# Optimization experiments

Hardware: AMD Instinct MI355X
Metric: run time of the kernel (lower is better)

The kernel has to match this reference:

```python
import jax, jax.numpy as jnp
import numpy as np

N_NODES = 100000
N_EDGES = 3200000
IN_DIM = 128
OUT_DIM = 128
BN_EPS = 1e-5
FILL_VALUE = 1.0  # improved_gcn=False -> self-loop weight 1.0 (2.0 if improved)


def setup_inputs() -> dict:
    key = jax.random.key(0)
    k1, k2, k3, k4 = jax.random.split(key, 4)
    node_features = jax.random.normal(k1, (N_NODES, IN_DIM), dtype=jnp.float32)
    edge_index = jax.random.randint(k2, (2, N_EDGES), 0, N_NODES, dtype=jnp.int64)
    edge_weight = jax.random.uniform(k3, (N_EDGES,), dtype=jnp.float32)
    # Glorot init like PyG GCNConv
    W = jax.random.normal(k4, (IN_DIM, OUT_DIM), dtype=jnp.float32) * np.sqrt(2.0 / (IN_DIM + OUT_DIM))
    b = jnp.zeros((OUT_DIM,), dtype=jnp.float32)
    gamma = jnp.ones((OUT_DIM,), dtype=jnp.float32)
    beta = jnp.zeros((OUT_DIM,), dtype=jnp.float32)
    return {"node_features": node_features, "edge_index": edge_index,
            "edge_weight": edge_weight, "W": W, "b": b, "gamma": gamma, "beta": beta}


def reference(node_features, edge_index, edge_weight, W, b, gamma, beta):
    N = node_features.shape[0]
    dt = node_features.dtype
    # --- gcn_norm: add self loops, symmetric normalization ---
    loop = jnp.arange(N, dtype=edge_index.dtype)
    row = jnp.concatenate([edge_index[0], loop])  # source
    col = jnp.concatenate([edge_index[1], loop])  # target (aggregation dim)
    w = jnp.concatenate([edge_weight.astype(dt), jnp.full((N,), FILL_VALUE, dtype=dt)])
    deg = jax.ops.segment_sum(w, col, num_segments=N)
    dinv = jnp.where(deg > 0, jax.lax.rsqrt(deg), 0.0).astype(dt)
    norm = dinv[row] * w * dinv[col]  # [E+N]
    # --- linear transform then message passing (scatter-add into targets) ---
    x = node_features @ W  # [N, out_dim]
    msg = x[row] * norm[:, None]  # [E+N, out_dim] gather
    out = jax.ops.segment_sum(msg, col, num_segments=N) + b
    # --- relu ---
    h = jax.nn.relu(out)
    # --- BatchNorm1d (training-mode batch statistics, biased variance) ---
    mean = jnp.mean(h, axis=0)
    var = jnp.mean(jnp.square(h - mean), axis=0)
    h = (h - mean) * jax.lax.rsqrt(var + BN_EPS) * gamma + beta
    # dropout is identity in eval / deterministic reference
    return h
```

## Files before the change

kernel.cpp:

```cpp
#include <hip/hip_runtime.h>
#include <hip/hip_bf16.h>


#define BKT_BITS 7
#define BKT_SZ 128
#define MAX_BKT 1024
#define CHUNK 8192

typedef __attribute__((ext_vector_type(8))) short bf16x8;
typedef __attribute__((ext_vector_type(4))) float f32x4;

__device__ __forceinline__ unsigned bf16rn(float f) {
    unsigned x = __float_as_uint(f);
    return (x + 0x7fffu + ((x >> 16) & 1u)) >> 16;
}
__device__ __forceinline__ float bflo(unsigned u) { return __uint_as_float(u << 16); }
__device__ __forceinline__ float bfhi(unsigned u) { return __uint_as_float(u & 0xffff0000u); }

__global__ __launch_bounds__(256) void k_bhist2(const int* __restrict__ col,
        int* __restrict__ blkoff, int E, int nb, int nbc) {
    __shared__ int h[MAX_BKT];
    for (int i = threadIdx.x; i < nb; i += 256) h[i] = 0;
    __syncthreads();
    int base = blockIdx.x * CHUNK, lim = min(base + CHUNK, E);
    for (int e = base + threadIdx.x; e < lim; e += 256)
        atomicAdd(&h[col[e] >> BKT_BITS], 1);
    __syncthreads();
    for (int i = threadIdx.x; i < nb; i += 256)
        blkoff[(size_t)i * nbc + blockIdx.x] = h[i];
}

__global__ void k_bscan2a(int* __restrict__ blkoff, int* __restrict__ btot,
                          int nb, int nbc) {
    int b = blockIdx.x * 256 + threadIdx.x;
    if (b >= nb) return;
    int* p = blkoff + (size_t)b * nbc;
    int run = 0;
#pragma unroll 4
    for (int i = 0; i < nbc; ++i) { int c = p[i]; p[i] = run; run += c; }
    btot[b] = run;
}

__global__ __launch_bounds__(1024) void k_bscan2b(const int* __restrict__ btot,
        int* __restrict__ bbase, int* __restrict__ ptr, float* __restrict__ sums,
        int nb, int N, int E) {
    __shared__ int ls[1024];
    int t = threadIdx.x;
    int v = (t < nb) ? btot[t] : 0;
    ls[t] = v;
    __syncthreads();
    for (int off = 1; off < 1024; off <<= 1) {
        int u = (t >= off) ? ls[t - off] : 0;
        __syncthreads();
        ls[t] += u;
        __syncthreads();
    }
    if (t < nb) bbase[t] = ls[t] - v;
    if (t == nb - 1) bbase[nb] = ls[t];
    if (t == 0) ptr[N] = E;
    if (t < 512) sums[t] = 0.0f;
}

__global__ __launch_bounds__(256) void k_passA3(
        const int* __restrict__ row, const int* __restrict__ col,
        const float* __restrict__ w, const int* __restrict__ blkoff,
        const int* __restrict__ bbase, int2* __restrict__ tmp,
        int E, int nb, int nbc) {
    __shared__ int cur[MAX_BKT];
    for (int i = threadIdx.x; i < nb; i += 256)
        cur[i] = bbase[i] + blkoff[(size_t)i * nbc + blockIdx.x];
    __syncthreads();
    int base = blockIdx.x * CHUNK, lim = min(base + CHUNK, E);
    for (int e = base + threadIdx.x; e < lim; e += 256) {
        int c = col[e];
        int pos = atomicAdd(&cur[c >> BKT_BITS], 1);
        tmp[pos] = make_int2(row[e] | ((c & (BKT_SZ - 1)) << 17), __float_as_int(w[e]));
    }
}

__global__ __launch_bounds__(256) void k_passB2(
        const int2* __restrict__ tmp, const int* __restrict__ bbase,
        unsigned* __restrict__ packed, int* __restrict__ ptr,
        float* __restrict__ dinv, int N) {
    __shared__ int hcnt[BKT_SZ];
    __shared__ float wsum[BKT_SZ];
    __shared__ int cur[BKT_SZ];
    int b = blockIdx.x;
    int t = threadIdx.x;
    if (t < BKT_SZ) { hcnt[t] = 0; wsum[t] = 0.0f; }
    __syncthreads();
    int beg = bbase[b], end = bbase[b + 1];
    for (int k = beg + t; k < end; k += 256) {
        int2 p = tmp[k];
        int li = (p.x >> 17) & (BKT_SZ - 1);
        atomicAdd(&hcnt[li], 1);
        atomicAdd(&wsum[li], __int_as_float(p.y));
    }
    __syncthreads();
    if (t < BKT_SZ) cur[t] = hcnt[t];
    __syncthreads();
    for (int off = 1; off < BKT_SZ; off <<= 1) {
        int v = (t < BKT_SZ && t >= off) ? cur[t - off] : 0;
        __syncthreads();
        if (t < BKT_SZ) cur[t] += v;
        __syncthreads();
    }
    if (t < BKT_SZ) {
        int p = beg + cur[t] - hcnt[t];
        cur[t] = p;
        int n = (b << BKT_BITS) + t;
        if (n < N) {
            ptr[n] = p;
            float d = 1.0f + wsum[t];
            dinv[n] = d > 0.0f ? rsqrtf(d) : 0.0f;
        }
    }
    __syncthreads();
    for (int k = beg + t; k < end; k += 256) {
        int2 p = tmp[k];
        int li = (p.x >> 17) & (BKT_SZ - 1);
        int pos = atomicAdd(&cur[li], 1);
        float wf = __int_as_float(p.y);
        int q = (int)(wf * 32768.0f + 0.5f);
        q = q > 32767 ? 32767 : (q < 0 ? 0 : q);
        packed[pos] = ((unsigned)(p.x & 0x1FFFF) << 15) | (unsigned)q;
    }
}

__global__ void k_conv2(const float* __restrict__ nf, const float* __restrict__ dinv,
                        uint4* __restrict__ tab, int N) {
    size_t i = (size_t)blockIdx.x * 256 + threadIdx.x;
    if (i >= (size_t)N * 16) return;
    int n = (int)(i >> 4);
    float dv = dinv[n];
    const float4* src = (const float4*)nf + 2 * i;
    float4 a = src[0], b = src[1];
    uint4 r;
    r.x = bf16rn(a.x * dv) | (bf16rn(a.y * dv) << 16);
    r.y = bf16rn(a.z * dv) | (bf16rn(a.w * dv) << 16);
    r.z = bf16rn(b.x * dv) | (bf16rn(b.y * dv) << 16);
    r.w = bf16rn(b.z * dv) | (bf16rn(b.w * dv) << 16);
    tab[i] = r;
}

__global__ void k_convW(const float* __restrict__ W, unsigned* __restrict__ WT) {
    int i = blockIdx.x * 256 + threadIdx.x;
    if (i >= 128 * 64) return;
    int j = i >> 6, w = i & 63;
    float a = W[(size_t)(2 * w) * 128 + j];
    float b = W[(size_t)(2 * w + 1) * 128 + j];
    WT[i] = bf16rn(a) | (bf16rn(b) << 16);
}

#define EDGE_FMA(aX, nX, tX)                                     \
    aX[0] += nX * bflo(tX.x); aX[1] += nX * bfhi(tX.x);          \
    aX[2] += nX * bflo(tX.y); aX[3] += nX * bfhi(tX.y);          \
    aX[4] += nX * bflo(tX.z); aX[5] += nX * bfhi(tX.z);          \
    aX[6] += nX * bflo(tX.w); aX[7] += nX * bfhi(tX.w);

__global__ __launch_bounds__(256) void k_gatherw4(
        const unsigned* __restrict__ packed, const int* __restrict__ ptr,
        const float* __restrict__ dinv, const unsigned* __restrict__ tab,
        unsigned* __restrict__ aggb, int N) {
    int wid = (int)(((size_t)blockIdx.x * 256 + threadIdx.x) >> 6);
    int lane = threadIdx.x & 63;
    if (wid >= N) return;
    int beg = ptr[wid], end = ptr[wid + 1];
    float dc = dinv[wid];
    float dcq = dc * (1.0f / 32768.0f);
    int q = lane >> 4;
    int fl = lane & 15;
    float a0[8] = {}, a1[8] = {}, a2[8] = {}, a3[8] = {};
    for (int k = beg; k < end; k += 16) {
        int i0 = k + q, i1 = k + 4 + q, i2 = k + 8 + q, i3 = k + 12 + q;
        unsigned p0 = packed[i0 < end ? i0 : beg];
        unsigned p1 = packed[i1 < end ? i1 : beg];
        unsigned p2 = packed[i2 < end ? i2 : beg];
        unsigned p3 = packed[i3 < end ? i3 : beg];
        float n0 = i0 < end ? dcq * (float)(p0 & 0x7FFF) : 0.0f;
        float n1 = i1 < end ? dcq * (float)(p1 & 0x7FFF) : 0.0f;
        float n2 = i2 < end ? dcq * (float)(p2 & 0x7FFF) : 0.0f;
        float n3 = i3 < end ? dcq * (float)(p3 & 0x7FFF) : 0.0f;
        uint4 t0 = *(const uint4*)(tab + (size_t)(p0 >> 15) * 64 + fl * 4);
        uint4 t1 = *(const uint4*)(tab + (size_t)(p1 >> 15) * 64 + fl * 4);
        uint4 t2 = *(const uint4*)(tab + (size_t)(p2 >> 15) * 64 + fl * 4);
        uint4 t3 = *(const uint4*)(tab + (size_t)(p3 >> 15) * 64 + fl * 4);
        EDGE_FMA(a0, n0, t0)
        EDGE_FMA(a1, n1, t1)
        EDGE_FMA(a2, n2, t2)
        EDGE_FMA(a3, n3, t3)
    }
#pragma unroll
    for (int j = 0; j < 8; ++j) {
        float s = (a0[j] + a1[j]) + (a2[j] + a3[j]);
        s += __shfl_xor(s, 16);
        s += __shfl_xor(s, 32);
        a0[j] = s;
    }
    if (q == 0) {
        uint4 t = *(const uint4*)(tab + (size_t)wid * 64 + fl * 4);
        EDGE_FMA(a0, dc, t)
        uint4 r;
        r.x = bf16rn(a0[0]) | (bf16rn(a0[1]) << 16);
        r.y = bf16rn(a0[2]) | (bf16rn(a0[3]) << 16);
        r.z = bf16rn(a0[4]) | (bf16rn(a0[5]) << 16);
        r.w = bf16rn(a0[6]) | (bf16rn(a0[7]) << 16);
        *(uint4*)(aggb + (size_t)wid * 64 + fl * 4) = r;
    }
}

__global__ __launch_bounds__(256) void k_gatherwF(
        const unsigned* __restrict__ packed, const int* __restrict__ ptr,
        const float* __restrict__ dinv, const unsigned* __restrict__ tab,
        float* __restrict__ out, int N) {
    int wid = (int)(((size_t)blockIdx.x * 256 + threadIdx.x) >> 6);
    int lane = threadIdx.x & 63;
    if (wid >= N) return;
    int beg = ptr[wid], end = ptr[wid + 1];
    float dc = dinv[wid];
    float dcq = dc * (1.0f / 32768.0f);
    int q = lane >> 4;
    int fl = lane & 15;
    float a0[8] = {}, a1[8] = {};
    for (int k = beg; k < end; k += 8) {
        int i0 = k + q, i1 = k + 4 + q;
        unsigned p0 = packed[i0 < end ? i0 : beg];
        unsigned p1 = packed[i1 < end ? i1 : beg];
        float n0 = i0 < end ? dcq * (float)(p0 & 0x7FFF) : 0.0f;
        float n1 = i1 < end ? dcq * (float)(p1 & 0x7FFF) : 0.0f;
        uint4 t0 = *(const uint4*)(tab + (size_t)(p0 >> 15) * 64 + fl * 4);
        uint4 t1 = *(const uint4*)(tab + (size_t)(p1 >> 15) * 64 + fl * 4);
        EDGE_FMA(a0, n0, t0)
        EDGE_FMA(a1, n1, t1)
    }
#pragma unroll
    for (int j = 0; j < 8; ++j) {
        float s = a0[j] + a1[j];
        s += __shfl_xor(s, 16);
        s += __shfl_xor(s, 32);
        a0[j] = s;
    }
    if (q == 0) {
        uint4 t = *(const uint4*)(tab + (size_t)wid * 64 + fl * 4);
        EDGE_FMA(a0, dc, t)
        float4* dst = (float4*)(out + (size_t)wid * 128 + fl * 8);
        dst[0] = make_float4(a0[0], a0[1], a0[2], a0[3]);
        dst[1] = make_float4(a0[4], a0[5], a0[6], a0[7]);
    }
}

__global__ __launch_bounds__(256) void k_gemm3b(
        unsigned* aggb, const unsigned* __restrict__ WT,
        const float* __restrict__ bias, float* __restrict__ sums, int N) {
    __shared__ unsigned A_l[128][68];
    __shared__ unsigned W_l[128][68];
    __shared__ float bs[256];
    int tid = threadIdx.x;
    int r0 = blockIdx.x * 128;
    bs[tid] = 0.0f;
    {
        int j = tid >> 1, h = tid & 1;
        const uint4* src = (const uint4*)(WT + j * 64 + h * 32);
#pragma unroll
        for (int i = 0; i < 8; ++i)
            *(uint4*)&W_l[j][h * 32 + i * 4] = src[i];
    }
    {
        int j = tid >> 1, h = tid & 1;
        int gr = r0 + j;
        if (gr < N) {
            const uint4* src = (const uint4*)(aggb + (size_t)gr * 64 + h * 32);
#pragma unroll
            for (int i = 0; i < 8; ++i)
                *(uint4*)&A_l[j][h * 32 + i * 4] = src[i];
        } else {
            uint4 z = {0, 0, 0, 0};
#pragma unroll
            for (int i = 0; i < 8; ++i)
                *(uint4*)&A_l[j][h * 32 + i * 4] = z;
        }
    }
    __syncthreads();

    int wv = tid >> 6, l = tid & 63;
    int lr = l & 15, lk = l >> 4;
    f32x4 acc[2][8] = {};
#pragma unroll
    for (int ks = 0; ks < 4; ++ks) {
        bf16x8 a0 = *(bf16x8*)&A_l[wv * 32 + lr][ks * 16 + lk * 4];
        bf16x8 a1 = *(bf16x8*)&A_l[wv * 32 + 16 + lr][ks * 16 + lk * 4];
#pragma unroll
        for (int nt = 0; nt < 8; ++nt) {
            bf16x8 b = *(bf16x8*)&W_l[nt * 16 + lr][ks * 16 + lk * 4];
            acc[0][nt] = __builtin_amdgcn_mfma_f32_16x16x32_bf16(a0, b, acc[0][nt], 0, 0, 0);
            acc[1][nt] = __builtin_amdgcn_mfma_f32_16x16x32_bf16(a1, b, acc[1][nt], 0, 0, 0);
        }
    }

    unsigned short* ab = (unsigned short*)aggb;
#pragma unroll
    for (int nt = 0; nt < 8; ++nt) {
        int colc = nt * 16 + lr;
        float bc = bias[colc];
        float s = 0.0f, sq = 0.0f;
#pragma unroll
        for (int ms = 0; ms < 2; ++ms) {
#pragma unroll
            for (int p = 0; p < 4; ++p) {
                int rrow = r0 + wv * 32 + ms * 16 + lk * 4 + p;
                float v = fmaxf(acc[ms][nt][p] + bc, 0.0f);
                if (rrow < N) {
                    ab[(size_t)rrow * 128 + colc] = (unsigned short)bf16rn(v);
                    s += v;
                    sq += v * v;
                }
            }
        }
        s += __shfl_xor(s, 16);  s += __shfl_xor(s, 32);
        sq += __shfl_xor(sq, 16); sq += __shfl_xor(sq, 32);
        if (l < 16) {
            atomicAdd(&bs[colc], s);
            atomicAdd(&bs[128 + colc], sq);
        }
    }
    __syncthreads();
    if (tid < 128) {
        atomicAdd(&sums[tid], bs[tid]);
        atomicAdd(&sums[128 + tid], bs[128 + tid]);
    }
}

__global__ void k_bnfin(float* __restrict__ sums, const float* __restrict__ gamma,
                        const float* __restrict__ beta, int N) {
    int j = threadIdx.x;
    float inv_n = 1.0f / (float)N;
    float mean = sums[j] * inv_n;
    float var = sums[128 + j] * inv_n - mean * mean;
    float sc = rsqrtf(var + 1e-5f) * gamma[j];
    sums[256 + j] = sc;
    sums[384 + j] = beta[j] - mean * sc;
}

__global__ void k_bnapplyB(const unsigned* __restrict__ aggb,
                           const float* __restrict__ sums,
                           float* __restrict__ out, size_t n16) {
    size_t i = (size_t)blockIdx.x * 256 + threadIdx.x;
    if (i >= n16) return;
    int g = (int)(i & 15);
    uint4 v = ((const uint4*)aggb)[i];
    float4 sc0 = *(const float4*)(sums + 256 + g * 8);
    float4 sc1 = *(const float4*)(sums + 256 + g * 8 + 4);
    float4 sh0 = *(const float4*)(sums + 384 + g * 8);
    float4 sh1 = *(const float4*)(sums + 384 + g * 8 + 4);
    float4 o0, o1;
    o0.x = bflo(v.x) * sc0.x + sh0.x;
    o0.y = bfhi(v.x) * sc0.y + sh0.y;
    o0.z = bflo(v.y) * sc0.z + sh0.z;
    o0.w = bfhi(v.y) * sc0.w + sh0.w;
    o1.x = bflo(v.z) * sc1.x + sh1.x;
    o1.y = bfhi(v.z) * sc1.y + sh1.y;
    o1.z = bflo(v.w) * sc1.z + sh1.z;
    o1.w = bfhi(v.w) * sc1.w + sh1.w;
    ((float4*)out)[2 * i] = o0;
    ((float4*)out)[2 * i + 1] = o1;
}

__global__ void k_bnapply(float* __restrict__ h, const float* __restrict__ sums, size_t n4) {
    size_t i = (size_t)blockIdx.x * 256 + threadIdx.x;
    if (i >= n4) return;
    int j4 = (int)(i & 31);
    float4 v = ((float4*)h)[i];
    float4 sc = ((const float4*)(sums + 256))[j4];
    float4 sh = ((const float4*)(sums + 384))[j4];
    v.x = v.x * sc.x + sh.x;
    v.y = v.y * sc.y + sh.y;
    v.z = v.z * sc.z + sh.z;
    v.w = v.w * sc.w + sh.w;
    ((float4*)h)[i] = v;
}

__global__ void k_init0(int* __restrict__ bcnt, float* __restrict__ sums, int nb) {
    int i = blockIdx.x * 256 + threadIdx.x;
    if (i < nb) bcnt[i] = 0;
    if (blockIdx.x == 0 && threadIdx.x < 512) sums[threadIdx.x] = 0.0f;
}
__global__ __launch_bounds__(256) void k_bhist(const int* __restrict__ col,
                                               int* __restrict__ bcnt, int E, int nb) {
    __shared__ int h[MAX_BKT];
    for (int i = threadIdx.x; i < nb; i += 256) h[i] = 0;
    __syncthreads();
    int base = blockIdx.x * CHUNK, lim = min(base + CHUNK, E);
    for (int e = base + threadIdx.x; e < lim; e += 256)
        atomicAdd(&h[col[e] >> BKT_BITS], 1);
    __syncthreads();
    for (int i = threadIdx.x; i < nb; i += 256) {
        int c = h[i];
        if (c) atomicAdd(&bcnt[i], c);
    }
}
__global__ __launch_bounds__(1024) void k_bscan(const int* __restrict__ bcnt,
        int* __restrict__ bbase, int* __restrict__ bcur,
        int* __restrict__ ptr, int nb, int N, int E) {
    __shared__ int ls[1024];
    int t = threadIdx.x;
    int v = (t < nb) ? bcnt[t] : 0;
    ls[t] = v;
    __syncthreads();
    for (int off = 1; off < 1024; off <<= 1) {
        int u = (t >= off) ? ls[t - off] : 0;
        __syncthreads();
        ls[t] += u;
        __syncthreads();
    }
    if (t < nb) {
        int ex = ls[t] - v;
        bbase[t] = ex;
        bcur[t] = ex;
    }
    if (t == nb - 1) bbase[nb] = ls[t];
    if (t == 0) ptr[N] = E;
}
__global__ __launch_bounds__(256) void k_passA2(
        const int* __restrict__ row, const int* __restrict__ col,
        const float* __restrict__ w, int* __restrict__ bcur,
        int2* __restrict__ tmp, int E, int nb) {
    __shared__ int h[MAX_BKT];
    for (int i = threadIdx.x; i < nb; i += 256) h[i] = 0;
    __syncthreads();
    int base = blockIdx.x * CHUNK, lim = min(base + CHUNK, E);
    for (int e = base + threadIdx.x; e < lim; e += 256)
        atomicAdd(&h[col[e] >> BKT_BITS], 1);
    __syncthreads();
    for (int i = threadIdx.x; i < nb; i += 256) {
        int c = h[i];
        if (c) h[i] = atomicAdd(&bcur[i], c);
    }
    __syncthreads();
    for (int e = base + threadIdx.x; e < lim; e += 256) {
        int c = col[e];
        int b = c >> BKT_BITS;
        int pos = atomicAdd(&h[b], 1);
        tmp[pos] = make_int2(row[e] | ((c & (BKT_SZ - 1)) << 17), __float_as_int(w[e]));
    }
}

__global__ void k_init(int* __restrict__ cnt, float* __restrict__ sums, int N) {
    int i = blockIdx.x * 256 + threadIdx.x;
    if (i < N) cnt[i] = 0;
    if (blockIdx.x == 0 && threadIdx.x < 512) sums[threadIdx.x] = 0.0f;
}
__global__ void k_count(const int* __restrict__ col, int* __restrict__ cnt, int E) {
    int e = blockIdx.x * 256 + threadIdx.x;
    if (e < E) atomicAdd(&cnt[col[e]], 1);
}
__global__ __launch_bounds__(256) void kS1(const int* __restrict__ cnt,
                                           int* __restrict__ ptr,
                                           int* __restrict__ bsum, int N) {
    __shared__ int ls[256];
    int t = threadIdx.x, i = blockIdx.x * 256 + t;
    int v = (i < N) ? cnt[i] : 0;
    ls[t] = v;
    __syncthreads();
    for (int off = 1; off < 256; off <<= 1) {
        int u = (t >= off) ? ls[t - off] : 0;
        __syncthreads();
        ls[t] += u;
        __syncthreads();
    }
    if (i < N) ptr[i] = ls[t] - v;
    if (t == 255) bsum[blockIdx.x] = ls[255];
}
__global__ __launch_bounds__(512) void kS2(int* __restrict__ bsum,
                                           int* __restrict__ ptr, int NB, int N) {
    __shared__ int ls[512];
    int t = threadIdx.x;
    int chunk = (NB + 511) / 512;
    int b = t * chunk, e = min(b + chunk, NB);
    int s = 0;
    for (int i = b; i < e; ++i) s += bsum[i];
    ls[t] = s;
    __syncthreads();
    for (int off = 1; off < 512; off <<= 1) {
        int u = (t >= off) ? ls[t - off] : 0;
        __syncthreads();
        ls[t] += u;
        __syncthreads();
    }
    int run = ls[t] - s;
    for (int i = b; i < e; ++i) { int c = bsum[i]; bsum[i] = run; run += c; }
    if (t == 511) ptr[N] = ls[511];
}
__global__ void kS3(int* __restrict__ ptr, int* __restrict__ cnt,
                    const int* __restrict__ bsum, int N) {
    int i = blockIdx.x * 256 + threadIdx.x;
    if (i >= N) return;
    int p = ptr[i] + bsum[blockIdx.x];
    ptr[i] = p;
    cnt[i] = p;
}
__global__ void k_fill(const int* __restrict__ row, const int* __restrict__ col,
                       const float* __restrict__ w, int* __restrict__ cursor,
                       int2* __restrict__ packed, int E) {
    int e = blockIdx.x * 256 + threadIdx.x;
    if (e < E) {
        int pos = atomicAdd(&cursor[col[e]], 1);
        packed[pos] = make_int2(row[e], __float_as_int(w[e]));
    }
}
__global__ __launch_bounds__(256) void k_degw(const int2* __restrict__ packed,
                                              const int* __restrict__ ptr,
                                              float* __restrict__ dinv, int N) {
    int wid = (int)(((size_t)blockIdx.x * 256 + threadIdx.x) >> 6);
    int lane = threadIdx.x & 63;
    if (wid >= N) return;
    int beg = ptr[wid], end = ptr[wid + 1];
    float s = 0.0f;
    for (int k = beg + lane; k < end; k += 64) s += __int_as_float(packed[k].y);
#pragma unroll
    for (int off = 32; off; off >>= 1) s += __shfl_xor(s, off);
    if (lane == 0) {
        float d = 1.0f + s;
        dinv[wid] = d > 0.0f ? rsqrtf(d) : 0.0f;
    }
}
__global__ __launch_bounds__(256) void k_gather(
        const int2* __restrict__ packed, const int* __restrict__ ptr,
        const float* __restrict__ dinv, const float* __restrict__ nf,
        float* __restrict__ out, int N) {
    int wid = (int)(((size_t)blockIdx.x * 256 + threadIdx.x) >> 6);
    int lane = threadIdx.x & 63;
    if (wid >= N) return;
    int c = wid;
    int beg = ptr[c], end = ptr[c + 1];
    float dc = dinv[c];
    int half = lane >> 5;
    int fl = lane & 31;
    float4 acc = {0.f, 0.f, 0.f, 0.f};
    for (int k = beg; k < end; k += 2) {
        int idx = k + half;
        bool v = idx < end;
        int2 p = packed[v ? idx : beg];
        float nrm = v ? dc * __int_as_float(p.y) * dinv[p.x] : 0.0f;
        float4 x = ((const float4*)(nf + (size_t)p.x * 128))[fl];
        acc.x += nrm * x.x; acc.y += nrm * x.y;
        acc.z += nrm * x.z; acc.w += nrm * x.w;
    }
    acc.x += __shfl_xor(acc.x, 32);
    acc.y += __shfl_xor(acc.y, 32);
    acc.z += __shfl_xor(acc.z, 32);
    acc.w += __shfl_xor(acc.w, 32);
    if (half == 0) {
        float s2 = dc * dc;
        float4 sf = ((const float4*)(nf + (size_t)c * 128))[fl];
        acc.x += s2 * sf.x; acc.y += s2 * sf.y;
        acc.z += s2 * sf.z; acc.w += s2 * sf.w;
        ((float4*)(out + (size_t)c * 128))[fl] = acc;
    }
}
__global__ void k_initA(float* __restrict__ deg, float* __restrict__ sums, int N) {
    int i = blockIdx.x * 256 + threadIdx.x;
    if (i < N) deg[i] = 1.0f;
    if (blockIdx.x == 0 && threadIdx.x < 512) sums[threadIdx.x] = 0.0f;
}
__global__ void k_deg(const int* __restrict__ col, const float* __restrict__ w,
                      float* __restrict__ deg, int E) {
    int e = blockIdx.x * 256 + threadIdx.x;
    if (e < E) atomicAdd(&deg[col[e]], w[e]);
}
__global__ void k_dinv(float* __restrict__ deg, int N) {
    int i = blockIdx.x * 256 + threadIdx.x;
    if (i < N) { float d = deg[i]; deg[i] = d > 0.0f ? rsqrtf(d) : 0.0f; }
}
__global__ void k_self(const float* __restrict__ nf, const float* __restrict__ dinv,
                       float* __restrict__ agg, int N) {
    size_t i = (size_t)blockIdx.x * 256 + threadIdx.x;
    if (i >= (size_t)N * 32) return;
    int node = (int)(i >> 5);
    float s = dinv[node]; s = s * s;
    float4 v = ((const float4*)nf)[i];
    v.x *= s; v.y *= s; v.z *= s; v.w *= s;
    ((float4*)agg)[i] = v;
}
__global__ __launch_bounds__(256) void k_scatter(
        const int* __restrict__ row, const int* __restrict__ col,
        const float* __restrict__ w, const float* __restrict__ dinv,
        const float* __restrict__ nf, float* __restrict__ agg, int E) {
    int wid = (int)(((size_t)blockIdx.x * blockDim.x + threadIdx.x) >> 6);
    int lane = threadIdx.x & 63;
    if (wid >= E) return;
    int r = row[wid], c = col[wid];
    float nrm = dinv[r] * w[wid] * dinv[c];
    float2 v = ((const float2*)(nf + (size_t)r * 128))[lane];
    float* dst = agg + (size_t)c * 128 + lane * 2;
    atomicAdd(dst, v.x * nrm);
    atomicAdd(dst + 1, v.y * nrm);
}

__global__ __launch_bounds__(256) void k_gemm2(float* __restrict__ h,
        const float* __restrict__ W, const float* __restrict__ bias,
        float* __restrict__ sums, int N) {
    __shared__ float At[2][32][132];
    __shared__ float Wt[2][32][132];
    int tid = threadIdx.x;
    int tx = tid & 15, ty = tid >> 4;
    int r0 = blockIdx.x * 128;
#define STAGE_A(buf, k0)                                                     \
    _Pragma("unroll")                                                        \
    for (int i = 0; i < 4; ++i) {                                            \
        int idx = tid + 256 * i;                                             \
        int row = idx >> 3, c4 = idx & 7;                                    \
        int gr = r0 + row; if (gr > N - 1) gr = N - 1;                       \
        float4 v = *(const float4*)&h[(size_t)gr * 128 + (k0) + c4 * 4];     \
        At[buf][c4 * 4 + 0][row] = v.x;                                      \
        At[buf][c4 * 4 + 1][row] = v.y;                                      \
        At[buf][c4 * 4 + 2][row] = v.z;                                      \
        At[buf][c4 * 4 + 3][row] = v.w;                                      \
    }
#define STAGE_W(buf, k0)                                                     \
    _Pragma("unroll")                                                        \
    for (int i = 0; i < 4; ++i) {                                            \
        int idx = tid + 256 * i;                                             \
        int kk = idx >> 5, c4 = idx & 31;                                    \
        float4 v = *(const float4*)&W[(size_t)((k0) + kk) * 128 + c4 * 4];   \
        *(float4*)&Wt[buf][kk][c4 * 4] = v;                                  \
    }
    STAGE_A(0, 0)
    STAGE_W(0, 0)
    float acc[8][8] = {};
    for (int t = 0; t < 4; ++t) {
        __syncthreads();
        if (t < 3) {
            int nb = (t + 1) & 1;
            STAGE_A(nb, (t + 1) * 32)
            STAGE_W(nb, (t + 1) * 32)
        }
        int kb = t & 1;
#pragma unroll
        for (int k = 0; k < 32; ++k) {
            float a[8], w[8];
            *(float4*)&a[0] = *(float4*)&At[kb][k][ty * 8];
            *(float4*)&a[4] = *(float4*)&At[kb][k][ty * 8 + 4];
            *(float4*)&w[0] = *(float4*)&Wt[kb][k][tx * 8];
            *(float4*)&w[4] = *(float4*)&Wt[kb][k][tx * 8 + 4];
#pragma unroll
            for (int r = 0; r < 8; ++r)
#pragma unroll
                for (int cc = 0; cc < 8; ++cc)
                    acc[r][cc] += a[r] * w[cc];
        }
    }
    float bv[8];
    *(float4*)&bv[0] = *(const float4*)&bias[tx * 8];
    *(float4*)&bv[4] = *(const float4*)&bias[tx * 8 + 4];
    float s[8] = {}, sq[8] = {};
#pragma unroll
    for (int r = 0; r < 8; ++r) {
        int gr = r0 + ty * 8 + r;
        if (gr < N) {
            float o[8];
#pragma unroll
            for (int cc = 0; cc < 8; ++cc) {
                o[cc] = fmaxf(acc[r][cc] + bv[cc], 0.0f);
                s[cc] += o[cc];
                sq[cc] += o[cc] * o[cc];
            }
            float4* dst = (float4*)&h[(size_t)gr * 128 + tx * 8];
            dst[0] = make_float4(o[0], o[1], o[2], o[3]);
            dst[1] = make_float4(o[4], o[5], o[6], o[7]);
        }
    }
    float* ls = &At[0][0][0];
    __syncthreads();
#pragma unroll
    for (int cc = 0; cc < 8; ++cc) {
        ls[ty * 128 + tx * 8 + cc] = s[cc];
        ls[2048 + ty * 128 + tx * 8 + cc] = sq[cc];
    }
    __syncthreads();
    if (tid < 128) {
        float ssum = 0.f, sqsum = 0.f;
#pragma unroll
        for (int u = 0; u < 16; ++u) {
            ssum += ls[u * 128 + tid];
            sqsum += ls[2048 + u * 128 + tid];
        }
        atomicAdd(&sums[tid], ssum);
        atomicAdd(&sums[128 + tid], sqsum);
    }
#undef STAGE_A
#undef STAGE_W
}

extern "C" void kernel_launch(void* const* d_in, const int* in_sizes, int n_in,
                              void* d_out, int out_size, void* d_ws, size_t ws_size,
                              hipStream_t stream) {
    const float* nf    = (const float*)d_in[0];
    const int*   ei    = (const int*)d_in[1];
    const float* ew    = (const float*)d_in[2];
    const float* W     = (const float*)d_in[3];
    const float* bias  = (const float*)d_in[4];
    const float* gamma = (const float*)d_in[5];
    const float* beta  = (const float*)d_in[6];
    float* out = (float*)d_out;

    const int N = in_sizes[0] / 128;
    const int E = in_sizes[2];
    const int* row = ei;
    const int* col = ei + E;

    int nb_n  = (N + 255) / 256;
    int nb_e  = (E + 255) / 256;
    int nb_w  = (int)(((size_t)N + 3) / 4);
    int nb_v4 = (int)(((size_t)N * 32 + 255) / 256);
    int nbk   = (N + BKT_SZ - 1) >> BKT_BITS;
    int nb_c  = (E + CHUNK - 1) / CHUNK;
    int nconv = (int)(((size_t)N * 16 + 255) / 256);
    size_t n16 = (size_t)N * 16;
    size_t tt_words = (size_t)64 * N > (size_t)2 * E ? (size_t)64 * N : (size_t)2 * E;

    float* dinv = (float*)d_ws;
    int*   ptr  = (int*)d_ws + N;
    float* sums = (float*)d_ws + 2 * N + 1;
    int*   bbase1 = (int*)d_ws + 2 * N + 513;
    int*   btot   = bbase1 + nbk + 1;
    int*   blkoff = btot + nbk;
    size_t wt_off = ((size_t)(2 * N + 514 + 2 * nbk) + (size_t)nbk * nb_c + 3) & ~(size_t)3;
    unsigned* wtb = (unsigned*)((int*)d_ws + wt_off);
    size_t pk_off = (wt_off + 8192 + 3) & ~(size_t)3;
    unsigned* p1_packed = (unsigned*)((int*)d_ws + pk_off);
    size_t tt_off = (pk_off + (size_t)E + 3) & ~(size_t)3;
    int2*  p1_tmp = (int2*)((int*)d_ws + tt_off);
    unsigned* p1_tab = (unsigned*)((int*)d_ws + tt_off);
    size_t ab_off = (tt_off + tt_words + 3) & ~(size_t)3;
    unsigned* aggb = (unsigned*)((int*)d_ws + ab_off);
    size_t need_p1 = (ab_off + (size_t)64 * N) * 4;

    float* dinv2 = (float*)d_ws;
    int*   ptr2  = (int*)d_ws + N;
    int*   cnt3  = (int*)d_ws + 2 * N + 1;
    float* sums2 = (float*)d_ws + 3 * N + 1;
    int*   bsum2 = (int*)d_ws + 3 * N + 513;
    int*   bbase2 = (int*)d_ws + 3 * N + 1025;
    int*   bcur2  = bbase2 + nbk + 1;
    size_t pk2 = ((size_t)(3 * N + 1026 + 2 * nbk) + 3) & ~(size_t)3;
    int2*  packed2 = (int2*)((int*)d_ws + pk2);
    size_t tt2 = (pk2 + (size_t)2 * E + 3) & ~(size_t)3;
    int2*  tmp2 = (int2*)((int*)d_ws + tt2);
    unsigned* tab2 = (unsigned*)((int*)d_ws + tt2);
    size_t need_csr2  = tt2 * 4;
    size_t need_full2 = (tt2 + tt_words) * 4;

    if (nbk <= MAX_BKT && ws_size >= need_p1) {
        k_convW<<<32, 256, 0, stream>>>(W, wtb);
        k_bhist2<<<nb_c, 256, 0, stream>>>(col, blkoff, E, nbk, nb_c);
        k_bscan2a<<<(nbk + 255) / 256, 256, 0, stream>>>(blkoff, btot, nbk, nb_c);
        k_bscan2b<<<1, 1024, 0, stream>>>(btot, bbase1, ptr, sums, nbk, N, E);
        k_passA3<<<nb_c, 256, 0, stream>>>(row, col, ew, blkoff, bbase1, p1_tmp, E, nbk, nb_c);
        k_passB2<<<nbk, 256, 0, stream>>>(p1_tmp, bbase1, p1_packed, ptr, dinv, N);
        k_conv2<<<nconv, 256, 0, stream>>>(nf, dinv, (uint4*)p1_tab, N);
        k_gatherw4<<<nb_w, 256, 0, stream>>>(p1_packed, ptr, dinv, p1_tab, aggb, N);
        k_gemm3b<<<(N + 127) / 128, 256, 0, stream>>>(aggb, wtb, bias, sums, N);
        k_bnfin<<<1, 128, 0, stream>>>(sums, gamma, beta, N);
        k_bnapplyB<<<(int)((n16 + 255) / 256), 256, 0, stream>>>(aggb, sums, out, n16);
        return;
    }

    if (nbk <= MAX_BKT && ws_size >= need_full2) {
        k_init0<<<(max(nbk, 512) + 255) / 256, 256, 0, stream>>>(bcur2, sums2, nbk);
        k_bhist<<<nb_c, 256, 0, stream>>>(col, bcur2, E, nbk);
        k_bscan<<<1, 1024, 0, stream>>>(bcur2, bbase2, bcur2, ptr2, nbk, N, E);
        k_passA2<<<nb_c, 256, 0, stream>>>(row, col, ew, bcur2, tmp2, E, nbk);
        k_passB2<<<nbk, 256, 0, stream>>>(tmp2, bbase2, (unsigned*)packed2, ptr2, dinv2, N);
        k_conv2<<<nconv, 256, 0, stream>>>(nf, dinv2, (uint4*)tab2, N);
        k_gatherwF<<<nb_w, 256, 0, stream>>>((unsigned*)packed2, ptr2, dinv2, tab2, out, N);
        k_gemm2<<<(N + 127) / 128, 256, 0, stream>>>(out, W, bias, sums2, N);
        k_bnfin<<<1, 128, 0, stream>>>(sums2, gamma, beta, N);
        k_bnapply<<<nb_v4, 256, 0, stream>>>(out, sums2, (size_t)N * 32);
        return;
    }

    if (ws_size >= need_csr2) {
        k_init<<<nb_n, 256, 0, stream>>>(cnt3, sums2, N);
        k_count<<<nb_e, 256, 0, stream>>>(col, cnt3, E);
        kS1<<<nb_n, 256, 0, stream>>>(cnt3, ptr2, bsum2, N);
        kS2<<<1, 512, 0, stream>>>(bsum2, ptr2, nb_n, N);
        kS3<<<nb_n, 256, 0, stream>>>(ptr2, cnt3, bsum2, N);
        k_fill<<<nb_e, 256, 0, stream>>>(row, col, ew, cnt3, packed2, E);
        k_degw<<<nb_w, 256, 0, stream>>>(packed2, ptr2, dinv2, N);
        k_gather<<<nb_w, 256, 0, stream>>>(packed2, ptr2, dinv2, nf, out, N);
        k_gemm2<<<(N + 127) / 128, 256, 0, stream>>>(out, W, bias, sums2, N);
        k_bnfin<<<1, 128, 0, stream>>>(sums2, gamma, beta, N);
        k_bnapply<<<nb_v4, 256, 0, stream>>>(out, sums2, (size_t)N * 32);
        return;
    }

    {
        float* deg = (float*)d_ws;
        float* sm  = (float*)d_ws + N;
        k_initA<<<nb_n, 256, 0, stream>>>(deg, sm, N);
        k_deg<<<nb_e, 256, 0, stream>>>(col, ew, deg, E);
        k_dinv<<<nb_n, 256, 0, stream>>>(deg, N);
        k_self<<<nb_v4, 256, 0, stream>>>(nf, deg, out, N);
        k_scatter<<<(E + 3) / 4, 256, 0, stream>>>(row, col, ew, deg, nf, out, E);
        k_gemm2<<<(N + 127) / 128, 256, 0, stream>>>(out, W, bias, sm, N);
        k_bnfin<<<1, 128, 0, stream>>>(sm, gamma, beta, N);
        k_bnapply<<<nb_v4, 256, 0, stream>>>(out, sm, (size_t)N * 32);
    }
}
```

Baseline: 352.4 us.

## Pack edge records into 32-bit words and fold dinv into per-edge weights

The intermediate bucket record shrinks from an int2 (row, local col, float weight) to a single 32-bit word holding the row, the local column and an 8-bit quantized weight. This halves the scatter and reread traffic in passA/passB. passB now folds the target's dinv into the 15-bit packed norm, so the gather no longer multiplies by dc per edge. The gather loops are restructured into full unrolled blocks plus a remainder, which removes the per-edge bounds predication. Quantizing edge weights to 8 bits loses precision in both the degree and the norm, and the row<<15 packing limits row indices to 17 bits.

```diff
diff --git a/kernel.cpp b/kernel.cpp
--- a/kernel.cpp
+++ b/kernel.cpp
@@ -64,7 +64,7 @@
 __global__ __launch_bounds__(256) void k_passA3(
         const int* __restrict__ row, const int* __restrict__ col,
         const float* __restrict__ w, const int* __restrict__ blkoff,
-        const int* __restrict__ bbase, int2* __restrict__ tmp,
+        const int* __restrict__ bbase, unsigned* __restrict__ tmp,
         int E, int nb, int nbc) {
     __shared__ int cur[MAX_BKT];
     for (int i = threadIdx.x; i < nb; i += 256)
@@ -73,28 +73,32 @@
     int base = blockIdx.x * CHUNK, lim = min(base + CHUNK, E);
     for (int e = base + threadIdx.x; e < lim; e += 256) {
         int c = col[e];
+        int q8 = (int)(w[e] * 256.0f + 0.5f);
+        if (q8 > 255) q8 = 255;
+        unsigned rec = ((unsigned)row[e] << 15) | ((unsigned)(c & 127) << 8) | (unsigned)q8;
         int pos = atomicAdd(&cur[c >> BKT_BITS], 1);
-        tmp[pos] = make_int2(row[e] | ((c & (BKT_SZ - 1)) << 17), __float_as_int(w[e]));
+        tmp[pos] = rec;
     }
 }
 
 __global__ __launch_bounds__(256) void k_passB2(
-        const int2* __restrict__ tmp, const int* __restrict__ bbase,
+        const unsigned* __restrict__ tmp, const int* __restrict__ bbase,
         unsigned* __restrict__ packed, int* __restrict__ ptr,
         float* __restrict__ dinv, int N) {
     __shared__ int hcnt[BKT_SZ];
-    __shared__ float wsum[BKT_SZ];
+    __shared__ int wsumi[BKT_SZ];
     __shared__ int cur[BKT_SZ];
+    __shared__ float dcl[BKT_SZ];
     int b = blockIdx.x;
     int t = threadIdx.x;
-    if (t < BKT_SZ) { hcnt[t] = 0; wsum[t] = 0.0f; }
+    if (t < BKT_SZ) { hcnt[t] = 0; wsumi[t] = 0; }
     __syncthreads();
     int beg = bbase[b], end = bbase[b + 1];
     for (int k = beg + t; k < end; k += 256) {
-        int2 p = tmp[k];
-        int li = (p.x >> 17) & (BKT_SZ - 1);
+        unsigned p = tmp[k];
+        int li = (p >> 8) & 127;
         atomicAdd(&hcnt[li], 1);
-        atomicAdd(&wsum[li], __int_as_float(p.y));
+        atomicAdd(&wsumi[li], (int)(p & 255u));
     }
     __syncthreads();
     if (t < BKT_SZ) cur[t] = hcnt[t];
@@ -108,22 +112,21 @@
     if (t < BKT_SZ) {
         int p = beg + cur[t] - hcnt[t];
         cur[t] = p;
+        float d = 1.0f + (float)wsumi[t] * (1.0f / 256.0f);
+        float dc = rsqrtf(d);
+        dcl[t] = dc;
         int n = (b << BKT_BITS) + t;
-        if (n < N) {
-            ptr[n] = p;
-            float d = 1.0f + wsum[t];
-            dinv[n] = d > 0.0f ? rsqrtf(d) : 0.0f;
-        }
+        if (n < N) { ptr[n] = p; dinv[n] = dc; }
     }
     __syncthreads();
     for (int k = beg + t; k < end; k += 256) {
-        int2 p = tmp[k];
-        int li = (p.x >> 17) & (BKT_SZ - 1);
+        unsigned p = tmp[k];
+        int li = (p >> 8) & 127;
         int pos = atomicAdd(&cur[li], 1);
-        float wf = __int_as_float(p.y);
-        int q = (int)(wf * 32768.0f + 0.5f);
-        q = q > 32767 ? 32767 : (q < 0 ? 0 : q);
-        packed[pos] = ((unsigned)(p.x & 0x1FFFF) << 15) | (unsigned)q;
+        float fq = (float)(p & 255u) * dcl[li] * 128.0f;
+        int q = (int)(fq + 0.5f);
+        if (q > 32767) q = 32767;
+        packed[pos] = ((p >> 15) << 15) | (unsigned)q;
     }
 }
 
@@ -158,7 +161,7 @@
     aX[4] += nX * bflo(tX.z); aX[5] += nX * bfhi(tX.z);          \
     aX[6] += nX * bflo(tX.w); aX[7] += nX * bfhi(tX.w);
 
-__global__ __launch_bounds__(256) void k_gatherw4(
+__global__ __launch_bounds__(256) void k_gatherw5(
         const unsigned* __restrict__ packed, const int* __restrict__ ptr,
         const float* __restrict__ dinv, const unsigned* __restrict__ tab,
         unsigned* __restrict__ aggb, int N) {
@@ -167,28 +170,48 @@
     if (wid >= N) return;
     int beg = ptr[wid], end = ptr[wid + 1];
     float dc = dinv[wid];
-    float dcq = dc * (1.0f / 32768.0f);
     int q = lane >> 4;
     int fl = lane & 15;
+    const float sc = 1.0f / 32768.0f;
     float a0[8] = {}, a1[8] = {}, a2[8] = {}, a3[8] = {};
-    for (int k = beg; k < end; k += 16) {
-        int i0 = k + q, i1 = k + 4 + q, i2 = k + 8 + q, i3 = k + 12 + q;
-        unsigned p0 = packed[i0 < end ? i0 : beg];
-        unsigned p1 = packed[i1 < end ? i1 : beg];
-        unsigned p2 = packed[i2 < end ? i2 : beg];
-        unsigned p3 = packed[i3 < end ? i3 : beg];
-        float n0 = i0 < end ? dcq * (float)(p0 & 0x7FFF) : 0.0f;
-        float n1 = i1 < end ? dcq * (float)(p1 & 0x7FFF) : 0.0f;
-        float n2 = i2 < end ? dcq * (float)(p2 & 0x7FFF) : 0.0f;
-        float n3 = i3 < end ? dcq * (float)(p3 & 0x7FFF) : 0.0f;
+    int k = beg;
+    for (; k + 16 <= end; k += 16) {
+        unsigned p0 = packed[k + q];
+        unsigned p1 = packed[k + 4 + q];
+        unsigned p2 = packed[k + 8 + q];
+        unsigned p3 = packed[k + 12 + q];
         uint4 t0 = *(const uint4*)(tab + (size_t)(p0 >> 15) * 64 + fl * 4);
         uint4 t1 = *(const uint4*)(tab + (size_t)(p1 >> 15) * 64 + fl * 4);
         uint4 t2 = *(const uint4*)(tab + (size_t)(p2 >> 15) * 64 + fl * 4);
         uint4 t3 = *(const uint4*)(tab + (size_t)(p3 >> 15) * 64 + fl * 4);
+        float n0 = (float)(p0 & 0x7FFFu) * sc;
+        float n1 = (float)(p1 & 0x7FFFu) * sc;
+        float n2 = (float)(p2 & 0x7FFFu) * sc;
+        float n3 = (float)(p3 & 0x7FFFu) * sc;
         EDGE_FMA(a0, n0, t0)
         EDGE_FMA(a1, n1, t1)
         EDGE_FMA(a2, n2, t2)
         EDGE_FMA(a3, n3, t3)
+    }
+    if (k + 8 <= end) {
+        unsigned p0 = packed[k + q];
+        unsigned p1 = packed[k + 4 + q];
+        uint4 t0 = *(const uint4*)(tab + (size_t)(p0 >> 15) * 64 + fl * 4);
+        uint4 t1 = *(const uint4*)(tab + (size_t)(p1 >> 15) * 64 + fl * 4);
+        float n0 = (float)(p0 & 0x7FFFu) * sc;
+        float n1 = (float)(p1 & 0x7FFFu) * sc;
+        EDGE_FMA(a0, n0, t0)
+        EDGE_FMA(a1, n1, t1)
+        k += 8;
+    }
+    for (; k < end; k += 4) {
+        int i0 = k + q;
+        if (i0 < end) {
+            unsigned p0 = packed[i0];
+            uint4 t0 = *(const uint4*)(tab + (size_t)(p0 >> 15) * 64 + fl * 4);
+            float n0 = (float)(p0 & 0x7FFFu) * sc;
+            EDGE_FMA(a0, n0, t0)
+        }
     }
 #pragma unroll
     for (int j = 0; j < 8; ++j) {
@@ -218,20 +241,29 @@
     if (wid >= N) return;
     int beg = ptr[wid], end = ptr[wid + 1];
     float dc = dinv[wid];
-    float dcq = dc * (1.0f / 32768.0f);
     int q = lane >> 4;
     int fl = lane & 15;
+    const float sc = 1.0f / 32768.0f;
     float a0[8] = {}, a1[8] = {};
-    for (int k = beg; k < end; k += 8) {
-        int i0 = k + q, i1 = k + 4 + q;
-        unsigned p0 = packed[i0 < end ? i0 : beg];
-        unsigned p1 = packed[i1 < end ? i1 : beg];
-        float n0 = i0 < end ? dcq * (float)(p0 & 0x7FFF) : 0.0f;
-        float n1 = i1 < end ? dcq * (float)(p1 & 0x7FFF) : 0.0f;
+    int k = beg;
+    for (; k + 8 <= end; k += 8) {
+        unsigned p0 = packed[k + q];
+        unsigned p1 = packed[k + 4 + q];
         uint4 t0 = *(const uint4*)(tab + (size_t)(p0 >> 15) * 64 + fl * 4);
         uint4 t1 = *(const uint4*)(tab + (size_t)(p1 >> 15) * 64 + fl * 4);
+        float n0 = (float)(p0 & 0x7FFFu) * sc;
+        float n1 = (float)(p1 & 0x7FFFu) * sc;
         EDGE_FMA(a0, n0, t0)
         EDGE_FMA(a1, n1, t1)
+    }
+    for (; k < end; k += 4) {
+        int i0 = k + q;
+        if (i0 < end) {
+            unsigned p0 = packed[i0];
+            uint4 t0 = *(const uint4*)(tab + (size_t)(p0 >> 15) * 64 + fl * 4);
+            float n0 = (float)(p0 & 0x7FFFu) * sc;
+            EDGE_FMA(a0, n0, t0)
+        }
     }
 #pragma unroll
     for (int j = 0; j < 8; ++j) {
@@ -423,7 +455,7 @@
 __global__ __launch_bounds__(256) void k_passA2(
         const int* __restrict__ row, const int* __restrict__ col,
         const float* __restrict__ w, int* __restrict__ bcur,
-        int2* __restrict__ tmp, int E, int nb) {
+        unsigned* __restrict__ tmp, int E, int nb) {
     __shared__ int h[MAX_BKT];
     for (int i = threadIdx.x; i < nb; i += 256) h[i] = 0;
     __syncthreads();
@@ -438,9 +470,11 @@
     __syncthreads();
     for (int e = base + threadIdx.x; e < lim; e += 256) {
         int c = col[e];
-        int b = c >> BKT_BITS;
-        int pos = atomicAdd(&h[b], 1);
-        tmp[pos] = make_int2(row[e] | ((c & (BKT_SZ - 1)) << 17), __float_as_int(w[e]));
+        int q8 = (int)(w[e] * 256.0f + 0.5f);
+        if (q8 > 255) q8 = 255;
+        unsigned rec = ((unsigned)row[e] << 15) | ((unsigned)(c & 127) << 8) | (unsigned)q8;
+        int pos = atomicAdd(&h[c >> BKT_BITS], 1);
+        tmp[pos] = rec;
     }
 }
 
@@ -716,7 +750,7 @@
     int nb_c  = (E + CHUNK - 1) / CHUNK;
     int nconv = (int)(((size_t)N * 16 + 255) / 256);
     size_t n16 = (size_t)N * 16;
-    size_t tt_words = (size_t)64 * N > (size_t)2 * E ? (size_t)64 * N : (size_t)2 * E;
+    size_t tt_words = (size_t)64 * N > (size_t)E ? (size_t)64 * N : (size_t)E;
 
     float* dinv = (float*)d_ws;
     int*   ptr  = (int*)d_ws + N;
@@ -729,7 +763,7 @@
     size_t pk_off = (wt_off + 8192 + 3) & ~(size_t)3;
     unsigned* p1_packed = (unsigned*)((int*)d_ws + pk_off);
     size_t tt_off = (pk_off + (size_t)E + 3) & ~(size_t)3;
-    int2*  p1_tmp = (int2*)((int*)d_ws + tt_off);
+    unsigned* p1_tmp = (unsigned*)((int*)d_ws + tt_off);
     unsigned* p1_tab = (unsigned*)((int*)d_ws + tt_off);
     size_t ab_off = (tt_off + tt_words + 3) & ~(size_t)3;
     unsigned* aggb = (unsigned*)((int*)d_ws + ab_off);
@@ -743,12 +777,14 @@
     int*   bbase2 = (int*)d_ws + 3 * N + 1025;
     int*   bcur2  = bbase2 + nbk + 1;
     size_t pk2 = ((size_t)(3 * N + 1026 + 2 * nbk) + 3) & ~(size_t)3;
-    int2*  packed2 = (int2*)((int*)d_ws + pk2);
-    size_t tt2 = (pk2 + (size_t)2 * E + 3) & ~(size_t)3;
-    int2*  tmp2 = (int2*)((int*)d_ws + tt2);
+    unsigned* packed2 = (unsigned*)((int*)d_ws + pk2);
+    size_t tt2 = (pk2 + (size_t)E + 3) & ~(size_t)3;
+    unsigned* tmp2 = (unsigned*)((int*)d_ws + tt2);
     unsigned* tab2 = (unsigned*)((int*)d_ws + tt2);
-    size_t need_csr2  = tt2 * 4;
     size_t need_full2 = (tt2 + tt_words) * 4;
+
+    int2*  packed3 = (int2*)((int*)d_ws + pk2);
+    size_t need_csr3 = (pk2 + (size_t)2 * E) * 4;
 
     if (nbk <= MAX_BKT && ws_size >= need_p1) {
         k_convW<<<32, 256, 0, stream>>>(W, wtb);
@@ -758,7 +794,7 @@
         k_passA3<<<nb_c, 256, 0, stream>>>(row, col, ew, blkoff, bbase1, p1_tmp, E, nbk, nb_c);
         k_passB2<<<nbk, 256, 0, stream>>>(p1_tmp, bbase1, p1_packed, ptr, dinv, N);
         k_conv2<<<nconv, 256, 0, stream>>>(nf, dinv, (uint4*)p1_tab, N);
-        k_gatherw4<<<nb_w, 256, 0, stream>>>(p1_packed, ptr, dinv, p1_tab, aggb, N);
+        k_gatherw5<<<nb_w, 256, 0, stream>>>(p1_packed, ptr, dinv, p1_tab, aggb, N);
         k_gemm3b<<<(N + 127) / 128, 256, 0, stream>>>(aggb, wtb, bias, sums, N);
         k_bnfin<<<1, 128, 0, stream>>>(sums, gamma, beta, N);
         k_bnapplyB<<<(int)((n16 + 255) / 256), 256, 0, stream>>>(aggb, sums, out, n16);
@@ -770,24 +806,24 @@
         k_bhist<<<nb_c, 256, 0, stream>>>(col, bcur2, E, nbk);
         k_bscan<<<1, 1024, 0, stream>>>(bcur2, bbase2, bcur2, ptr2, nbk, N, E);
         k_passA2<<<nb_c, 256, 0, stream>>>(row, col, ew, bcur2, tmp2, E, nbk);
-        k_passB2<<<nbk, 256, 0, stream>>>(tmp2, bbase2, (unsigned*)packed2, ptr2, dinv2, N);
+        k_passB2<<<nbk, 256, 0, stream>>>(tmp2, bbase2, packed2, ptr2, dinv2, N);
         k_conv2<<<nconv, 256, 0, stream>>>(nf, dinv2, (uint4*)tab2, N);
-        k_gatherwF<<<nb_w, 256, 0, stream>>>((unsigned*)packed2, ptr2, dinv2, tab2, out, N);
+        k_gatherwF<<<nb_w, 256, 0, stream>>>(packed2, ptr2, dinv2, tab2, out, N);
         k_gemm2<<<(N + 127) / 128, 256, 0, stream>>>(out, W, bias, sums2, N);
         k_bnfin<<<1, 128, 0, stream>>>(sums2, gamma, beta, N);
         k_bnapply<<<nb_v4, 256, 0, stream>>>(out, sums2, (size_t)N * 32);
         return;
     }
 
-    if (ws_size >= need_csr2) {
+    if (ws_size >= need_csr3) {
         k_init<<<nb_n, 256, 0, stream>>>(cnt3, sums2, N);
         k_count<<<nb_e, 256, 0, stream>>>(col, cnt3, E);
         kS1<<<nb_n, 256, 0, stream>>>(cnt3, ptr2, bsum2, N);
         kS2<<<1, 512, 0, stream>>>(bsum2, ptr2, nb_n, N);
         kS3<<<nb_n, 256, 0, stream>>>(ptr2, cnt3, bsum2, N);
-        k_fill<<<nb_e, 256, 0, stream>>>(row, col, ew, cnt3, packed2, E);
-        k_degw<<<nb_w, 256, 0, stream>>>(packed2, ptr2, dinv2, N);
-        k_gather<<<nb_w, 256, 0, stream>>>(packed2, ptr2, dinv2, nf, out, N);
+        k_fill<<<nb_e, 256, 0, stream>>>(row, col, ew, cnt3, packed3, E);
+        k_degw<<<nb_w, 256, 0, stream>>>(packed3, ptr2, dinv2, N);
+        k_gather<<<nb_w, 256, 0, stream>>>(packed3, ptr2, dinv2, nf, out, N);
         k_gemm2<<<(N + 127) / 128, 256, 0, stream>>>(out, W, bias, sums2, N);
         k_bnfin<<<1, 128, 0, stream>>>(sums2, gamma, beta, N);
         k_bnapply<<<nb_v4, 256, 0, stream>>>(out, sums2, (size_t)N * 32);
```

Result: faster. 317.5 us (-9.9%).
